# Optimization experiments

Hardware: AMD Instinct MI355X
Metric: run time of the kernel (lower is better)

Reference implementation:

```python
import jax, jax.numpy as jnp
import numpy as np

N_HEAD = 16
WINDOW = 16  # fixed_window_size


def setup_inputs() -> dict:
    key = jax.random.key(0)
    k1, k2, k3 = jax.random.split(key, 3)
    B, T, C = 2, 2048, 1024
    x = jax.random.normal(k1, (B, T, C), dtype=jnp.float32)
    # torch Linear(C, 3C, bias=False): y = x @ W.T with W [3C, C].
    # We store the pre-transposed [C, 3C] matrix so y = x @ w_qkv.
    w_qkv = jax.random.normal(k2, (C, 3 * C), dtype=jnp.float32) * (1.0 / np.sqrt(C))
    w_proj = jax.random.normal(k3, (C, C), dtype=jnp.float32) * (1.0 / np.sqrt(C))
    return {"x": x, "w_qkv": w_qkv, "w_proj": w_proj}


def reference(x, w_qkv, w_proj):
    B, T, C = x.shape
    H, D = N_HEAD, C // N_HEAD
    qkv = x @ w_qkv  # [B, T, 3C]
    q, k, v = jnp.split(qkv, 3, axis=-1)
    # [B, T, C] -> [B, H, T, D]
    q, k, v = (t.reshape(B, T, H, D).transpose(0, 2, 1, 3) for t in (q, k, v))
    att = jnp.einsum("bhtd,bhsd->bhts", q, k) * (1.0 / np.sqrt(D))  # [B,H,T,T]
    # Mask exactly as the torch module builds it: tril ones, then zero where
    # col - row >= fixed_window_size (note: col-row, per the source).
    row = jnp.arange(T)[:, None]
    col = jnp.arange(T)[None, :]
    mask = (col <= row) & ~(col - row >= WINDOW)  # [T, T] bool
    att = jnp.where(mask[None, None, :, :], att, -jnp.inf)
    att = jax.nn.softmax(att, axis=-1)
    y = jnp.einsum("bhts,bhsd->bhtd", att, v)  # [B,H,T,D]
    y = y.transpose(0, 2, 1, 3).reshape(B, T, C)
    return y @ w_proj
```

## Files before the change

kernel.cpp:

```cpp
#include <hip/hip_runtime.h>
#include <stdint.h>

#define LOG2E 1.4426950408889634f
#define QSCALE 0.18033688011112042f

typedef __attribute__((ext_vector_type(8))) short bf16x8;
typedef __attribute__((ext_vector_type(4))) float f32x4;
typedef __attribute__((ext_vector_type(8))) unsigned short u16x8;

#define B_ 2
#define T_ 2048
#define C_ 1024
#define H_ 16
#define D_ 64
#define BT_ 4096
#define N3_ 3072

#if __has_builtin(__builtin_amdgcn_exp2f)
#define EXP2(x) __builtin_amdgcn_exp2f(x)
#else
#define EXP2(x) exp2f(x)
#endif

__device__ __forceinline__ unsigned short f2bf(float f) {
  union { float f; unsigned u; } x; x.f = f;
  return (unsigned short)((x.u + 0x7fffu + ((x.u >> 16) & 1u)) >> 16);
}
__device__ __forceinline__ float bf2f(unsigned short u) {
  union { unsigned u; float f; } x; x.u = ((unsigned)u) << 16;
  return x.f;
}
__device__ __forceinline__ unsigned f2u(float f) {
  union { float f; unsigned u; } x; x.f = f; return x.u;
}
__device__ __forceinline__ unsigned pack_bf2(float a, float b) {
  return __builtin_amdgcn_perm(f2u(b) + 0x8000u, f2u(a) + 0x8000u, 0x07060302u);
}

__device__ __forceinline__ void gld16(const unsigned short* g, unsigned short* l) {
  __builtin_amdgcn_global_load_lds(
      (const __attribute__((address_space(1))) unsigned int*)g,
      (__attribute__((address_space(3))) unsigned int*)l, 16, 0, 0);
}

__global__ void cvt_kernel(const float* __restrict__ in, unsigned short* __restrict__ out, int n) {
  int i = (blockIdx.x * blockDim.x + threadIdx.x) * 4;
  if (i >= n) return;
  float4 v = *(const float4*)(in + i);
  ushort4 o;
  o.x = f2bf(v.x); o.y = f2bf(v.y); o.z = f2bf(v.z); o.w = f2bf(v.w);
  *(ushort4*)(out + i) = o;
}

__global__ void tr_kernel(const float* __restrict__ in, unsigned short* __restrict__ out, int K, int N) {
  __shared__ unsigned short tile[32][33];
  int n0 = blockIdx.x * 32, k0 = blockIdx.y * 32;
  int tx = threadIdx.x, ty = threadIdx.y;
  tile[ty][tx] = f2bf(in[(size_t)(k0 + ty) * N + n0 + tx]);
  __syncthreads();
  out[(size_t)(n0 + ty) * K + k0 + tx] = tile[tx][ty];
}

template <int MODE>
__global__ __launch_bounds__(256) void gemm_kernel(
    const unsigned short* __restrict__ A, const unsigned short* __restrict__ Bt,
    unsigned short* __restrict__ qo, unsigned short* __restrict__ ko,
    unsigned short* __restrict__ vo, float* __restrict__ fo) {
  __shared__ unsigned short As[128 * 32];
  __shared__ unsigned short Bs[64 * 32];
  const int tid = threadIdx.x;
  const int wave = tid >> 6, lane = tid & 63;
  const int quad = lane >> 4, l16 = lane & 15;
  const int wm = (wave >> 1) * 64, wn = (wave & 1) * 32;
  const int m0 = blockIdx.y * 128, n0 = blockIdx.x * 64;

  const int arow = tid >> 2, ach = tid & 3;
  const unsigned short* Ag0 = A + (size_t)(m0 + arow) * 1024 + ach * 8;
  const unsigned short* Ag1 = Ag0 + (size_t)64 * 1024;
  const unsigned short* Bg = Bt + (size_t)(n0 + arow) * 1024 + ach * 8;
  unsigned short* AsW0 = As + tid * 8;
  unsigned short* AsW1 = As + (tid + 256) * 8;
  unsigned short* BsW = Bs + tid * 8;

  f32x4 acc[4][2] = {};

  for (int k = 0; k < 1024; k += 32) {
    __syncthreads();
    gld16(Ag0 + k, AsW0);
    gld16(Ag1 + k, AsW1);
    gld16(Bg + k, BsW);
    __syncthreads();
    bf16x8 af[4], bfr[2];
#pragma unroll
    for (int mi = 0; mi < 4; mi++)
      af[mi] = *(const bf16x8*)(As + (wm + mi * 16 + l16) * 32 + quad * 8);
#pragma unroll
    for (int ni = 0; ni < 2; ni++)
      bfr[ni] = *(const bf16x8*)(Bs + (wn + ni * 16 + l16) * 32 + quad * 8);
#pragma unroll
    for (int mi = 0; mi < 4; mi++)
#pragma unroll
      for (int ni = 0; ni < 2; ni++)
        acc[mi][ni] = __builtin_amdgcn_mfma_f32_16x16x32_bf16(af[mi], bfr[ni], acc[mi][ni], 0, 0, 0);
  }

  if (MODE == 0) {
    const int part = n0 >> 10;
    const int hh = (n0 >> 6) & 15;
#pragma unroll
    for (int mi = 0; mi < 4; mi++) {
#pragma unroll
      for (int r = 0; r < 4; r++) {
        const int m = m0 + wm + mi * 16 + quad * 4 + r;
        const int b = m >> 11, t = m & 2047;
#pragma unroll
        for (int ni = 0; ni < 2; ni++) {
          const int d = wn + ni * 16 + l16;
          float val = acc[mi][ni][r];
          if (part == 0) val *= QSCALE;
          const unsigned short bv = f2bf(val);
          if (part == 0)
            qo[((size_t)(b * H_ + hh) * T_ + t) * D_ + d] = bv;
          else if (part == 1)
            ko[((size_t)(b * H_ + hh) * T_ + t) * D_ + d] = bv;
          else
            vo[((size_t)(b * H_ + hh) * D_ + d) * T_ + t] = bv;
        }
      }
    }
  } else {
#pragma unroll
    for (int mi = 0; mi < 4; mi++)
#pragma unroll
      for (int r = 0; r < 4; r++) {
        const int m = m0 + wm + mi * 16 + quad * 4 + r;
#pragma unroll
        for (int ni = 0; ni < 2; ni++)
          fo[(size_t)m * 1024 + n0 + wn + ni * 16 + l16] = acc[mi][ni][r];
      }
  }
}

__global__ __launch_bounds__(256) void attn_kernel(
    const unsigned short* __restrict__ qb, const unsigned short* __restrict__ kb,
    const unsigned short* __restrict__ vb, unsigned short* __restrict__ yb,
    unsigned short* __restrict__ po, float* __restrict__ pl) {
  const int tid = threadIdx.x;
  const int wave = tid >> 6, lane = tid & 63;
  const int quad = lane >> 4, l16 = lane & 15;

  const int bid = blockIdx.x;
  const int bh = bid / 63;
  const int u = bid - bh * 63;
  int qs, c, nch;
  if (u < 11) { qs = u; c = 0; nch = 1; }
  else if (u < 33) { int v = u - 11; qs = 11 + (v >> 1); c = v & 1; nch = 2; }
  else { int v = u - 33; qs = 22 + v / 3; c = v % 3; nch = 3; }
  const int nt = qs + 1;
  const int j0 = c * nt / nch, j1 = (c + 1) * nt / nch;
  const int b = bh >> 4, h = bh & 15;

  __shared__ unsigned short Ks[64 * 64];
  __shared__ unsigned short Vt[64 * 64];
  __shared__ unsigned short Ps[4 * 16 * 68];
  unsigned short* Pw = Ps + wave * 16 * 68;

  const unsigned short* Qg = qb + (size_t)bh * T_ * D_;
  const unsigned short* Kg = kb + (size_t)bh * T_ * D_;
  const unsigned short* Vg = vb + (size_t)bh * D_ * T_;

  const unsigned short* qp = Qg + (size_t)(qs * 64 + wave * 16 + l16) * D_ + quad * 8;
  bf16x8 qf0 = *(const bf16x8*)qp, qf1 = *(const bf16x8*)(qp + 32);

  f32x4 o[4] = {};
  float lacc = 0.f;
  const int qglob = qs * 64 + wave * 16 + l16;
  const int sloc_base = quad * 4;

  const int trow = tid >> 3, tch = tid & 7;

  for (int jt = j0; jt < j1; jt++) {
    const int s0 = jt * 64;
    __syncthreads();
    {
      const int r0 = trow, r1 = trow + 32;
      gld16(Kg + (size_t)(s0 + r0) * D_ + ((tch ^ (r0 & 7)) * 8), Ks + r0 * 64 + tch * 8);
      gld16(Kg + (size_t)(s0 + r1) * D_ + ((tch ^ (r1 & 7)) * 8), Ks + r1 * 64 + tch * 8);
      gld16(Vg + (size_t)r0 * T_ + s0 + ((tch ^ (r0 & 7)) * 8), Vt + r0 * 64 + tch * 8);
      gld16(Vg + (size_t)r1 * T_ + s0 + ((tch ^ (r1 & 7)) * 8), Vt + r1 * 64 + tch * 8);
    }
    __syncthreads();

    f32x4 s[4];
#pragma unroll
    for (int mi = 0; mi < 4; mi++) {
      const int row = mi * 16 + l16, sw = row & 7;
      bf16x8 kf0 = *(const bf16x8*)(Ks + row * 64 + ((quad ^ sw) * 8));
      bf16x8 kf1 = *(const bf16x8*)(Ks + row * 64 + (((quad + 4) ^ sw) * 8));
      f32x4 z = {0.f, 0.f, 0.f, 0.f};
      z = __builtin_amdgcn_mfma_f32_16x16x32_bf16(kf0, qf0, z, 0, 0, 0);
      s[mi] = __builtin_amdgcn_mfma_f32_16x16x32_bf16(kf1, qf1, z, 0, 0, 0);
    }

    if (jt == qs) {
#pragma unroll
      for (int mi = 0; mi < 4; mi++)
#pragma unroll
        for (int r = 0; r < 4; r++) {
          float p = EXP2(s[mi][r]);
          p = (s0 + mi * 16 + sloc_base + r > qglob) ? 0.f : p;
          s[mi][r] = p;
          lacc += p;
        }
    } else {
#pragma unroll
      for (int mi = 0; mi < 4; mi++)
#pragma unroll
        for (int r = 0; r < 4; r++) {
          float p = EXP2(s[mi][r]);
          s[mi][r] = p;
          lacc += p;
        }
    }

#pragma unroll
    for (int mi = 0; mi < 4; mi++) {
      unsigned d0 = pack_bf2(s[mi][0], s[mi][1]);
      unsigned d1 = pack_bf2(s[mi][2], s[mi][3]);
      *(uint2*)(Pw + l16 * 68 + mi * 16 + quad * 4) = make_uint2(d0, d1);
    }

#pragma unroll
    for (int kk = 0; kk < 2; kk++) {
      bf16x8 pf = *(const bf16x8*)(Pw + l16 * 68 + kk * 32 + quad * 8);
#pragma unroll
      for (int ni = 0; ni < 4; ni++) {
        const int row = ni * 16 + l16, sw = row & 7;
        bf16x8 vf = *(const bf16x8*)(Vt + row * 64 + (((kk * 4 + quad) ^ sw) * 8));
        o[ni] = __builtin_amdgcn_mfma_f32_16x16x32_bf16(pf, vf, o[ni], 0, 0, 0);
      }
    }
  }

  lacc += __shfl_xor(lacc, 16, 64);
  lacc += __shfl_xor(lacc, 32, 64);
  float lr[4];
#pragma unroll
  for (int r = 0; r < 4; r++) lr[r] = __shfl(lacc, quad * 4 + r, 16);

  if (nch == 1) {
#pragma unroll
    for (int r = 0; r < 4; r++) {
      float inv = 1.0f / lr[r];
      int tq = qs * 64 + wave * 16 + quad * 4 + r;
#pragma unroll
      for (int ni = 0; ni < 4; ni++)
        yb[((size_t)(b * T_ + tq)) * 1024 + h * 64 + ni * 16 + l16] = f2bf(o[ni][r] * inv);
    }
  } else {
    const int slot = 52 * bh + ((qs <= 21) ? ((qs - 11) * 2 + c) : (22 + (qs - 22) * 3 + c));
    unsigned short* pob = po + (size_t)slot * 4096;
#pragma unroll
    for (int r = 0; r < 4; r++) {
      const int row64 = wave * 16 + quad * 4 + r;
#pragma unroll
      for (int ni = 0; ni < 4; ni++)
        pob[row64 * 64 + ni * 16 + l16] = f2bf(o[ni][r]);
      if (l16 == 0) pl[slot * 64 + row64] = lr[r];
    }
  }
}

__global__ __launch_bounds__(256) void reduce_kernel(
    const unsigned short* __restrict__ po, const float* __restrict__ pl,
    unsigned short* __restrict__ yb) {
  int idx = blockIdx.x * 256 + threadIdx.x;
  int bh = idx / 21504;
  int rem = idx - bh * 21504;
  int rr = rem >> 4, cg = rem & 15;
  int qs = 11 + (rr >> 6), row64 = rr & 63;
  int base, nch;
  if (qs <= 21) { base = (qs - 11) * 2; nch = 2; }
  else { base = 22 + (qs - 22) * 3; nch = 3; }
  int b = bh >> 4, h = bh & 15;
  float a0 = 0.f, a1 = 0.f, a2 = 0.f, a3 = 0.f, l = 0.f;
  for (int cc = 0; cc < nch; cc++) {
    int slot = 52 * bh + base + cc;
    const unsigned short* p = po + (size_t)slot * 4096 + row64 * 64 + cg * 4;
    ushort4 uv = *(const ushort4*)p;
    a0 += bf2f(uv.x); a1 += bf2f(uv.y); a2 += bf2f(uv.z); a3 += bf2f(uv.w);
    l += pl[slot * 64 + row64];
  }
  float inv = 1.0f / l;
  int tq = qs * 64 + row64;
  ushort4 w;
  w.x = f2bf(a0 * inv); w.y = f2bf(a1 * inv); w.z = f2bf(a2 * inv); w.w = f2bf(a3 * inv);
  *(ushort4*)(yb + ((size_t)(b * T_ + tq)) * 1024 + h * 64 + cg * 4) = w;
}

extern "C" void kernel_launch(void* const* d_in, const int* in_sizes, int n_in,
                              void* d_out, int out_size, void* d_ws, size_t ws_size,
                              hipStream_t stream) {
  const float* x = (const float*)d_in[0];
  const float* w_qkv = (const float*)d_in[1];
  const float* w_proj = (const float*)d_in[2];
  float* out = (float*)d_out;

  unsigned short* xb = (unsigned short*)d_ws;
  unsigned short* wprojT = xb + (size_t)BT_ * C_;
  unsigned short* qb = wprojT + (size_t)C_ * C_;
  unsigned short* kb = qb + (size_t)B_ * H_ * T_ * D_;
  unsigned short* vb = kb + (size_t)B_ * H_ * T_ * D_;
  unsigned short* wqkvT = vb + (size_t)B_ * H_ * T_ * D_;
  unsigned short* po = wqkvT;
  float* pl = (float*)(po + (size_t)1664 * 4096);
  unsigned short* yb = xb;

  cvt_kernel<<<(BT_ * C_ / 4 + 255) / 256, 256, 0, stream>>>(x, xb, BT_ * C_);
  dim3 trb(32, 32);
  tr_kernel<<<dim3(N3_ / 32, C_ / 32), trb, 0, stream>>>(w_qkv, wqkvT, C_, N3_);
  tr_kernel<<<dim3(C_ / 32, C_ / 32), trb, 0, stream>>>(w_proj, wprojT, C_, C_);

  gemm_kernel<0><<<dim3(N3_ / 64, BT_ / 128), 256, 0, stream>>>(xb, wqkvT, qb, kb, vb, nullptr);
  attn_kernel<<<dim3(32 * 63), 256, 0, stream>>>(qb, kb, vb, yb, po, pl);
  reduce_kernel<<<dim3(2688), 256, 0, stream>>>(po, pl, yb);
  gemm_kernel<1><<<dim3(C_ / 64, BT_ / 128), 256, 0, stream>>>(yb, wprojT, nullptr, nullptr, nullptr, out);
}
```

Before: 211.2 us.

## Double GEMM K-tile to 64 with XOR-swizzled shared memory layout

Raises the GEMM K-step from 32 to 64, which halves the number of barrier pairs and global-to-LDS load rounds per output tile. Shared tiles are stored with an XOR swizzle on the 16-byte chunk index to avoid LDS bank conflicts when waves read MFMA fragments. LDS use per block doubles, which may lower occupancy.

```diff
diff --git a/kernel.cpp b/kernel.cpp
--- a/kernel.cpp
+++ b/kernel.cpp
@@ -66,42 +66,50 @@
     const unsigned short* __restrict__ A, const unsigned short* __restrict__ Bt,
     unsigned short* __restrict__ qo, unsigned short* __restrict__ ko,
     unsigned short* __restrict__ vo, float* __restrict__ fo) {
-  __shared__ unsigned short As[128 * 32];
-  __shared__ unsigned short Bs[64 * 32];
+  __shared__ unsigned short As[128 * 64];
+  __shared__ unsigned short Bs[64 * 64];
   const int tid = threadIdx.x;
   const int wave = tid >> 6, lane = tid & 63;
   const int quad = lane >> 4, l16 = lane & 15;
   const int wm = (wave >> 1) * 64, wn = (wave & 1) * 32;
   const int m0 = blockIdx.y * 128, n0 = blockIdx.x * 64;
 
-  const int arow = tid >> 2, ach = tid & 3;
-  const unsigned short* Ag0 = A + (size_t)(m0 + arow) * 1024 + ach * 8;
-  const unsigned short* Ag1 = Ag0 + (size_t)64 * 1024;
-  const unsigned short* Bg = Bt + (size_t)(n0 + arow) * 1024 + ach * 8;
-  unsigned short* AsW0 = As + tid * 8;
-  unsigned short* AsW1 = As + (tid + 256) * 8;
-  unsigned short* BsW = Bs + tid * 8;
-
   f32x4 acc[4][2] = {};
 
-  for (int k = 0; k < 1024; k += 32) {
+  for (int k = 0; k < 1024; k += 64) {
     __syncthreads();
-    gld16(Ag0 + k, AsW0);
-    gld16(Ag1 + k, AsW1);
-    gld16(Bg + k, BsW);
+#pragma unroll
+    for (int i = 0; i < 4; i++) {
+      const int s = tid + 256 * i;
+      const int row = s >> 3, ch = s & 7;
+      gld16(A + (size_t)(m0 + row) * 1024 + k + ((ch ^ (row & 7)) * 8), As + s * 8);
+    }
+#pragma unroll
+    for (int i = 0; i < 2; i++) {
+      const int s = tid + 256 * i;
+      const int row = s >> 3, ch = s & 7;
+      gld16(Bt + (size_t)(n0 + row) * 1024 + k + ((ch ^ (row & 7)) * 8), Bs + s * 8);
+    }
     __syncthreads();
-    bf16x8 af[4], bfr[2];
-#pragma unroll
-    for (int mi = 0; mi < 4; mi++)
-      af[mi] = *(const bf16x8*)(As + (wm + mi * 16 + l16) * 32 + quad * 8);
-#pragma unroll
-    for (int ni = 0; ni < 2; ni++)
-      bfr[ni] = *(const bf16x8*)(Bs + (wn + ni * 16 + l16) * 32 + quad * 8);
-#pragma unroll
-    for (int mi = 0; mi < 4; mi++)
-#pragma unroll
-      for (int ni = 0; ni < 2; ni++)
-        acc[mi][ni] = __builtin_amdgcn_mfma_f32_16x16x32_bf16(af[mi], bfr[ni], acc[mi][ni], 0, 0, 0);
+#pragma unroll
+    for (int sub = 0; sub < 2; sub++) {
+      bf16x8 af[4], bfr[2];
+#pragma unroll
+      for (int mi = 0; mi < 4; mi++) {
+        const int row = wm + mi * 16 + l16;
+        af[mi] = *(const bf16x8*)(As + row * 64 + (((sub * 4 + quad) ^ (row & 7)) * 8));
+      }
+#pragma unroll
+      for (int ni = 0; ni < 2; ni++) {
+        const int row = wn + ni * 16 + l16;
+        bfr[ni] = *(const bf16x8*)(Bs + row * 64 + (((sub * 4 + quad) ^ (row & 7)) * 8));
+      }
+#pragma unroll
+      for (int mi = 0; mi < 4; mi++)
+#pragma unroll
+        for (int ni = 0; ni < 2; ni++)
+          acc[mi][ni] = __builtin_amdgcn_mfma_f32_16x16x32_bf16(af[mi], bfr[ni], acc[mi][ni], 0, 0, 0);
+    }
   }
 
   if (MODE == 0) {
```

After: 199.6 us. 1.06x faster.
